# Kernel tuning notes

Hardware: AMD Instinct MI355X
Metric: run time of the kernel (lower is better)

Reference implementation:

```python
import jax, jax.numpy as jnp
import numpy as np

B = 128        # graph pairs per batch
NPG = 512      # nodes per graph (equal-size graphs -> dense batch is a reshape)
D = 64         # input feature dim
DEG = 16       # avg degree
FILTERS = [64, 32, 16]
RDIM = 10      # resize_dim
CCH = 8        # conv channels per similarity image
MLP = [32, 16, 8, 4, 1]


def _make_edges(rng, n_graphs, npg, deg):
    E = n_graphs * npg * deg
    off = np.repeat(np.arange(n_graphs, dtype=np.int64) * npg, npg * deg)
    src = rng.integers(0, npg, E) + off
    dst = rng.integers(0, npg, E) + off
    return jnp.asarray(np.stack([src, dst]), dtype=jnp.int32)


def setup_inputs() -> dict:
    key = jax.random.key(0)
    ks = jax.random.split(key, 40)
    rng = np.random.default_rng(0)
    N = B * NPG
    inp = {}
    inp['x_i'] = jax.random.normal(ks[0], (N, D), jnp.float32)
    inp['x_j'] = jax.random.normal(ks[1], (N, D), jnp.float32)
    # GCN weights
    dims = [D] + FILTERS
    k = 2
    for li in range(3):
        fi, fo = dims[li], dims[li + 1]
        inp[f'gcn_w{li}'] = jax.random.normal(ks[k], (fi, fo), jnp.float32) / np.sqrt(fi); k += 1
        inp[f'gcn_b{li}'] = jnp.zeros((fo,), jnp.float32)
    # Conv filters: one Conv2d(1->CCH, 3x3, SAME) per GNN layer, OIHW kernels
    for li in range(3):
        inp[f'conv_w{li}'] = jax.random.normal(ks[k], (CCH, 1, 3, 3), jnp.float32) / 3.0; k += 1
        inp[f'conv_b{li}'] = jnp.zeros((CCH,), jnp.float32)
    # MLP (Linear-ReLU stack) + scoring layer
    mdims = [3 * CCH * RDIM * RDIM] + MLP
    for li in range(len(MLP)):
        fi, fo = mdims[li], mdims[li + 1]
        inp[f'mlp_w{li}'] = jax.random.normal(ks[k], (fi, fo), jnp.float32) / np.sqrt(fi); k += 1
        inp[f'mlp_b{li}'] = jnp.zeros((fo,), jnp.float32)
    inp['score_w'] = jax.random.normal(ks[k], (1, 1), jnp.float32); k += 1
    inp['score_b'] = jnp.zeros((1,), jnp.float32)
    # Graph structure (int constants)
    inp['edge_index_i'] = _make_edges(rng, B, NPG, DEG)
    inp['edge_index_j'] = _make_edges(rng, B, NPG, DEG)
    batch = jnp.asarray(np.repeat(np.arange(B, dtype=np.int64), NPG), dtype=jnp.int32)
    inp['batch_i'] = batch
    inp['batch_j'] = batch
    return inp


def _gcn(x, ei, w, b):
    # PyG GCNConv: A_hat = D^-1/2 (A + I) D^-1/2 ; out = A_hat (x W) + b
    src, dst = ei[0], ei[1]
    n = x.shape[0]
    xw = x @ w
    deg = jax.ops.segment_sum(jnp.ones(ei.shape[1], xw.dtype), dst, num_segments=n) + 1.0
    inv = jax.lax.rsqrt(deg)
    msg = xw[src] * (inv[src] * inv[dst])[:, None]
    agg = jax.ops.segment_sum(msg, dst, num_segments=n)
    return agg + xw * (inv * inv)[:, None] + b


def _forward(x_i, x_j, gcn_w0, gcn_b0, gcn_w1, gcn_b1, gcn_w2, gcn_b2,
             conv_w0, conv_b0, conv_w1, conv_b1, conv_w2, conv_b2,
             mlp_w0, mlp_b0, mlp_w1, mlp_b1, mlp_w2, mlp_b2, mlp_w3, mlp_b3, mlp_w4, mlp_b4,
             score_w, score_b, edge_index_i, edge_index_j):
    gws = [(gcn_w0, gcn_b0), (gcn_w1, gcn_b1), (gcn_w2, gcn_b2)]
    cvs = [(conv_w0, conv_b0), (conv_w1, conv_b1), (conv_w2, conv_b2)]
    embs = []
    for li, (w, b) in enumerate(gws):
        x_i = _gcn(x_i, edge_index_i, w, b)
        x_j = _gcn(x_j, edge_index_j, w, b)
        if li != len(gws) - 1:  # activation + dropout (eval mode -> identity)
            x_i = jax.nn.relu(x_i)
            x_j = jax.nn.relu(x_j)
        h_i = x_i.reshape(B, NPG, -1)  # to_dense_batch (equal-size graphs)
        h_j = x_j.reshape(B, NPG, -1)
        sim = jnp.einsum('bnd,bmd->bnm', h_i, h_j)  # [B, NPG, NPG]
        simr = jax.image.resize(sim, (B, RDIM, RDIM), method='bilinear', antialias=False)
        cw, cb = cvs[li]
        y = jax.lax.conv_general_dilated(simr[:, None], cw, (1, 1), 'SAME')
        y = jax.nn.relu(y + cb[None, :, None, None])  # [B, CCH, RDIM, RDIM]
        embs.append(y.reshape(B, -1))
    feat = jnp.concatenate(embs, axis=1)  # [B, 3*CCH*RDIM*RDIM]
    for w, b in [(mlp_w0, mlp_b0), (mlp_w1, mlp_b1), (mlp_w2, mlp_b2), (mlp_w3, mlp_b3), (mlp_w4, mlp_b4)]:
        feat = jax.nn.relu(feat @ w + b)
    score = jax.nn.sigmoid(feat @ score_w + score_b)
    return score.reshape(-1)


def reference(x_i, x_j, gcn_w0, gcn_b0, gcn_w1, gcn_b1, gcn_w2, gcn_b2,
              conv_w0, conv_b0, conv_w1, conv_b1, conv_w2, conv_b2,
              mlp_w0, mlp_b0, mlp_w1, mlp_b1, mlp_w2, mlp_b2, mlp_w3, mlp_b3, mlp_w4, mlp_b4,
              score_w, score_b, edge_index_i, edge_index_j, batch_i, batch_j):
    # batch_i/batch_j are implicit in the block layout (equal-size graphs)
    return _forward(x_i, x_j, gcn_w0, gcn_b0, gcn_w1, gcn_b1, gcn_w2, gcn_b2,
                    conv_w0, conv_b0, conv_w1, conv_b1, conv_w2, conv_b2,
                    mlp_w0, mlp_b0, mlp_w1, mlp_b1, mlp_w2, mlp_b2, mlp_w3, mlp_b3, mlp_w4, mlp_b4,
                    score_w, score_b, edge_index_i, edge_index_j)
```

## Files before the change

kernel.cpp:

```cpp
#include <hip/hip_runtime.h>

typedef float fvec4 __attribute__((ext_vector_type(4)));

#define NN 65536
#define EE 1048576
#define BB 128
#define NPG 512
#define EPG 8192

__global__ __launch_bounds__(512)
void k_all(const float* __restrict__ x_i, const float* __restrict__ x_j,
           const float* __restrict__ gw0, const float* __restrict__ gb0,
           const float* __restrict__ gw1, const float* __restrict__ gb1,
           const float* __restrict__ gw2, const float* __restrict__ gb2,
           const int* __restrict__ ei, const int* __restrict__ ej,
           float* __restrict__ hs0, float* __restrict__ hs1, float* __restrict__ hs2) {
  __shared__ fvec4 bufA[NPG * 8];
  __shared__ fvec4 bufB[NPG * 8];
  __shared__ unsigned short sids[EPG];
  __shared__ int cnt[NPG];
  __shared__ int posb[NPG];
  __shared__ int nodeOf[NPG];
  __shared__ int bins[64];
  __shared__ int binpos[64];
  __shared__ int wsum[8];
  unsigned short* const dsts = reinterpret_cast<unsigned short*>(bufA);

  const int side = blockIdx.x >> 7;
  const int g = blockIdx.x & 127;
  const float* __restrict__ x = side ? x_j : x_i;
  const int* __restrict__ eidx = side ? ej : ei;
  const int v = threadIdx.x;
  const int base = g * NPG;
  const int ebase = g * EPG;

  cnt[v] = 0;
  if (v < 64) bins[v] = 0;
  __syncthreads();
  for (int k = v; k < EPG; k += 512) {
    int d = eidx[EE + ebase + k] - base;
    dsts[k] = (unsigned short)d;
    atomicAdd(&cnt[d], 1);
  }
  __syncthreads();

  const int count = cnt[v];
  const int deg = count > 63 ? 63 : count;
  atomicAdd(&bins[deg], 1);
  int xa = count;
  const int lane = v & 63;
#pragma unroll
  for (int d = 1; d < 64; d <<= 1) {
    int y = __shfl_up(xa, d, 64);
    if (lane >= d) xa += y;
  }
  const int wid = v >> 6;
  if (lane == 63) wsum[wid] = xa;
  __syncthreads();
  if (v < 64) {
    if (v == 0) {
      int a = 0;
#pragma unroll
      for (int i = 0; i < 8; ++i) { int tv = wsum[i]; wsum[i] = a; a += tv; }
    }
    int c = bins[v];
    int xb = c;
#pragma unroll
    for (int d = 1; d < 64; d <<= 1) {
      int y = __shfl_up(xb, d, 64);
      if (v >= d) xb += y;
    }
    binpos[v] = xb - c;
  }
  __syncthreads();
  const int start_v = xa - count + wsum[wid];
  posb[v] = start_v;
  {
    int rank = atomicAdd(&binpos[deg], 1);
    nodeOf[rank] = v;
  }
  __syncthreads();

  for (int k = v; k < EPG; k += 512) {
    int lv = eidx[ebase + k] - base;
    int p = atomicAdd(&posb[dsts[k]], 1);
    sids[p] = (unsigned short)((lv << 3) | (lv & 7));
  }
  __syncthreads();

  const int node = nodeOf[v];
  const int ncount = cnt[node];
  const int nstart = posb[node] - ncount;
  const float inv_v = rsqrtf((float)ncount + 1.0f);
  const int myKey = (node << 3) | (node & 7);

  constexpr int srows[20] = {25, 26, 76, 77, 127, 128, 178, 179, 229, 230,
                             281, 282, 332, 333, 383, 384, 434, 435, 485, 486};
  int slot = -1;
#pragma unroll
  for (int i = 0; i < 20; ++i)
    if (node == srows[i]) slot = i;
  const int hb = (side * BB + g) * 20;

  fvec4 a0[16];
#pragma unroll
  for (int q = 0; q < 16; ++q) a0[q] = fvec4{0.f, 0.f, 0.f, 0.f};
  {
    const fvec4* xv = reinterpret_cast<const fvec4*>(x + (size_t)(base + node) * 64);
#pragma unroll 1
    for (int k16 = 0; k16 < 4; ++k16) {
      fvec4 xq[4];
#pragma unroll
      for (int u = 0; u < 4; ++u) xq[u] = xv[4 * k16 + u];
#pragma unroll
      for (int u = 0; u < 4; ++u) {
#pragma unroll
        for (int j = 0; j < 4; ++j) {
          const float xk = xq[u][j];
          const fvec4* wr = reinterpret_cast<const fvec4*>(gw0 + (size_t)(16 * k16 + 4 * u + j) * 64);
#pragma unroll
          for (int q = 0; q < 16; ++q) a0[q] += xk * wr[q];
        }
      }
    }
  }

  fvec4 sA[8], sB[8];
#pragma unroll
  for (int q = 0; q < 8; ++q) {
    fvec4 mA = a0[q] * inv_v;
    fvec4 mB = a0[8 + q] * inv_v;
    bufA[myKey ^ q] = mA;
    bufB[myKey ^ q] = mB;
    sA[q] = mA;
    sB[q] = mB;
  }
  __syncthreads();

  {
    const int end = nstart + ncount;
    for (int e = nstart; e < end; ++e) {
      const int K = sids[e];
#pragma unroll
      for (int q = 0; q < 8; ++q) {
        const int idx = K ^ q;
        sA[q] += bufA[idx];
        sB[q] += bufB[idx];
      }
    }
  }

  fvec4 y1[8];
#pragma unroll
  for (int p = 0; p < 8; ++p) y1[p] = fvec4{0.f, 0.f, 0.f, 0.f};
  {
    const fvec4* gb0v = reinterpret_cast<const fvec4*>(gb0);
    fvec4* hp = reinterpret_cast<fvec4*>(hs0 + ((size_t)hb + slot) * 64);
#pragma unroll
    for (int q = 0; q < 16; ++q) {
      fvec4 s = (q < 8) ? sA[q] : sB[q - 8];
      fvec4 o = s * inv_v + gb0v[q];
#pragma unroll
      for (int j = 0; j < 4; ++j) o[j] = fmaxf(o[j], 0.f);
      if (slot >= 0) hp[q] = o;
#pragma unroll
      for (int j = 0; j < 4; ++j) {
        const float hf = o[j];
        const fvec4* wr = reinterpret_cast<const fvec4*>(gw1 + (size_t)(q * 4 + j) * 32);
#pragma unroll
        for (int p = 0; p < 8; ++p) y1[p] += hf * wr[p];
      }
    }
  }
  __syncthreads();

  fvec4 s1[8];
#pragma unroll
  for (int q = 0; q < 8; ++q) {
    fvec4 mv = y1[q] * inv_v;
    bufA[myKey ^ q] = mv;
    s1[q] = mv;
  }
  __syncthreads();
  {
    const int end = nstart + ncount;
    for (int e = nstart; e < end; ++e) {
      const int K = sids[e];
#pragma unroll
      for (int q = 0; q < 8; ++q) s1[q] += bufA[K ^ q];
    }
  }
  fvec4 y2[4];
#pragma unroll
  for (int p = 0; p < 4; ++p) y2[p] = fvec4{0.f, 0.f, 0.f, 0.f};
  {
    const fvec4* gb1v = reinterpret_cast<const fvec4*>(gb1);
    fvec4* hp = reinterpret_cast<fvec4*>(hs1 + ((size_t)hb + slot) * 32);
#pragma unroll
    for (int q = 0; q < 8; ++q) {
      fvec4 o = s1[q] * inv_v + gb1v[q];
#pragma unroll
      for (int j = 0; j < 4; ++j) o[j] = fmaxf(o[j], 0.f);
      if (slot >= 0) hp[q] = o;
#pragma unroll
      for (int j = 0; j < 4; ++j) {
        const float hf = o[j];
        const fvec4* wr = reinterpret_cast<const fvec4*>(gw2 + (size_t)(q * 4 + j) * 16);
#pragma unroll
        for (int p = 0; p < 4; ++p) y2[p] += hf * wr[p];
      }
    }
  }

  fvec4 s2[4];
#pragma unroll
  for (int q = 0; q < 4; ++q) {
    fvec4 mv = y2[q] * inv_v;
    bufB[myKey ^ q] = mv;
    s2[q] = mv;
  }
  __syncthreads();
  if (slot >= 0) {
    const int end = nstart + ncount;
    for (int e = nstart; e < end; ++e) {
      const int K = sids[e];
#pragma unroll
      for (int q = 0; q < 4; ++q) s2[q] += bufB[K ^ q];
    }
    const fvec4* gb2v = reinterpret_cast<const fvec4*>(gb2);
    fvec4* hp = reinterpret_cast<fvec4*>(hs2 + ((size_t)hb + slot) * 16);
#pragma unroll
    for (int q = 0; q < 4; ++q) hp[q] = s2[q] * inv_v + gb2v[q];
  }
}

__global__ __launch_bounds__(256) void k_head(const float* __restrict__ hs0, const float* __restrict__ hs1,
                                              const float* __restrict__ hs2,
                                              const float* __restrict__ cw0, const float* __restrict__ cb0,
                                              const float* __restrict__ cw1, const float* __restrict__ cb1,
                                              const float* __restrict__ cw2, const float* __restrict__ cb2,
                                              const float* __restrict__ mw0, const float* __restrict__ mb0,
                                              const float* __restrict__ mw1, const float* __restrict__ mb1,
                                              const float* __restrict__ mw2, const float* __restrict__ mb2,
                                              const float* __restrict__ mw3, const float* __restrict__ mb3,
                                              const float* __restrict__ mw4, const float* __restrict__ mb4,
                                              const float* __restrict__ sw, const float* __restrict__ sb,
                                              float* __restrict__ out) {
  __shared__ float hi[2240];
  __shared__ float hj[2240];
  __shared__ float sim[400];
  __shared__ float simr[100];
  __shared__ float feat[2400];
  __shared__ float red[256];
  __shared__ float mbuf[60];
  const int b = blockIdx.x, t = threadIdx.x;

  for (int k = t; k < 1280; k += 256) {
    hi[k] = hs0[(size_t)(0 * BB + b) * 1280 + k];
    hj[k] = hs0[(size_t)(1 * BB + b) * 1280 + k];
  }
  for (int k = t; k < 640; k += 256) {
    hi[1280 + k] = hs1[(size_t)(0 * BB + b) * 640 + k];
    hj[1280 + k] = hs1[(size_t)(1 * BB + b) * 640 + k];
  }
  for (int k = t; k < 320; k += 256) {
    hi[1920 + k] = hs2[(size_t)(0 * BB + b) * 320 + k];
    hj[1920 + k] = hs2[(size_t)(1 * BB + b) * 320 + k];
  }
  __syncthreads();

  const int Fs[3] = {64, 32, 16};
  const int HOFF[3] = {0, 1280, 1920};
  const float* CW[3] = {cw0, cw1, cw2};
  const float* CB[3] = {cb0, cb1, cb2};

  for (int li = 0; li < 3; ++li) {
    const int F = Fs[li];
    const float* Hi = hi + HOFF[li];
    const float* Hj = hj + HOFF[li];
    for (int p = t; p < 400; p += 256) {
      int r = p / 20, cq = p % 20;
      float a = 0.0f;
      for (int d = 0; d < F; ++d) a += Hi[r * F + d] * Hj[cq * F + d];
      sim[p] = a;
    }
    __syncthreads();
    if (t < 100) {
      int oy = t / 10, ox = t % 10;
      float cy = (oy + 0.5f) * (512.0f / 10.0f) - 0.5f;
      float cx = (ox + 0.5f) * (512.0f / 10.0f) - 0.5f;
      float fy = cy - floorf(cy);
      float fx = cx - floorf(cx);
      int r0 = 2 * oy, c0 = 2 * ox;
      float s00 = sim[r0 * 20 + c0], s01 = sim[r0 * 20 + c0 + 1];
      float s10 = sim[(r0 + 1) * 20 + c0], s11 = sim[(r0 + 1) * 20 + c0 + 1];
      simr[t] = (1.0f - fy) * ((1.0f - fx) * s00 + fx * s01) + fy * ((1.0f - fx) * s10 + fx * s11);
    }
    __syncthreads();
    const float* cw = CW[li];
    const float* cb = CB[li];
    for (int idx = t; idx < 800; idx += 256) {
      int cch = idx / 100, rem = idx % 100, y = rem / 10, x = rem % 10;
      float a = cb[cch];
#pragma unroll
      for (int ky = 0; ky < 3; ++ky) {
#pragma unroll
        for (int kx = 0; kx < 3; ++kx) {
          int iy = y + ky - 1, ix = x + kx - 1;
          if (iy >= 0 && iy < 10 && ix >= 0 && ix < 10)
            a += cw[cch * 9 + ky * 3 + kx] * simr[iy * 10 + ix];
        }
      }
      feat[li * 800 + idx] = fmaxf(a, 0.0f);
    }
    __syncthreads();
  }

  {
    int f = t & 31, part = t >> 5;
    float a = 0.0f;
    int k0 = part * 300;
    for (int k = k0; k < k0 + 300; ++k) a += feat[k] * mw0[k * 32 + f];
    red[t] = a;
    __syncthreads();
    if (t < 32) {
      float s = mb0[t];
#pragma unroll
      for (int p = 0; p < 8; ++p) s += red[p * 32 + t];
      mbuf[t] = fmaxf(s, 0.0f);
    }
    __syncthreads();
  }
  if (t < 16) {
    float s = mb1[t];
    for (int k = 0; k < 32; ++k) s += mbuf[k] * mw1[k * 16 + t];
    mbuf[32 + t] = fmaxf(s, 0.0f);
  }
  __syncthreads();
  if (t < 8) {
    float s = mb2[t];
    for (int k = 0; k < 16; ++k) s += mbuf[32 + k] * mw2[k * 8 + t];
    mbuf[48 + t] = fmaxf(s, 0.0f);
  }
  __syncthreads();
  if (t < 4) {
    float s = mb3[t];
    for (int k = 0; k < 8; ++k) s += mbuf[48 + k] * mw3[k * 4 + t];
    mbuf[56 + t] = fmaxf(s, 0.0f);
  }
  __syncthreads();
  if (t == 0) {
    float s = mb4[0];
    for (int k = 0; k < 4; ++k) s += mbuf[56 + k] * mw4[k];
    s = fmaxf(s, 0.0f);
    float z = s * sw[0] + sb[0];
    out[b] = 1.0f / (1.0f + expf(-z));
  }
}

extern "C" void kernel_launch(void* const* d_in, const int* in_sizes, int n_in,
                              void* d_out, int out_size, void* d_ws, size_t ws_size,
                              hipStream_t stream) {
  (void)in_sizes; (void)n_in; (void)out_size; (void)ws_size;
  const float* x_i = (const float*)d_in[0];
  const float* x_j = (const float*)d_in[1];
  const float* gw0 = (const float*)d_in[2];
  const float* gb0 = (const float*)d_in[3];
  const float* gw1 = (const float*)d_in[4];
  const float* gb1 = (const float*)d_in[5];
  const float* gw2 = (const float*)d_in[6];
  const float* gb2 = (const float*)d_in[7];
  const float* cw0 = (const float*)d_in[8];
  const float* cb0 = (const float*)d_in[9];
  const float* cw1 = (const float*)d_in[10];
  const float* cb1 = (const float*)d_in[11];
  const float* cw2 = (const float*)d_in[12];
  const float* cb2 = (const float*)d_in[13];
  const float* mw0 = (const float*)d_in[14];
  const float* mb0 = (const float*)d_in[15];
  const float* mw1 = (const float*)d_in[16];
  const float* mb1 = (const float*)d_in[17];
  const float* mw2 = (const float*)d_in[18];
  const float* mb2 = (const float*)d_in[19];
  const float* mw3 = (const float*)d_in[20];
  const float* mb3 = (const float*)d_in[21];
  const float* mw4 = (const float*)d_in[22];
  const float* mb4 = (const float*)d_in[23];
  const float* scw = (const float*)d_in[24];
  const float* scb = (const float*)d_in[25];
  const int* ei = (const int*)d_in[26];
  const int* ej = (const int*)d_in[27];
  float* out = (float*)d_out;

  char* p = (char*)d_ws;
  auto take = [&](size_t bytes) {
    char* r = p;
    p += (bytes + 255) & ~(size_t)255;
    return r;
  };
  float* hs0 = (float*)take((size_t)2 * BB * 20 * 64 * 4);
  float* hs1 = (float*)take((size_t)2 * BB * 20 * 32 * 4);
  float* hs2 = (float*)take((size_t)2 * BB * 20 * 16 * 4);

  k_all<<<2 * BB, 512, 0, stream>>>(x_i, x_j, gw0, gb0, gw1, gb1, gw2, gb2,
                                    ei, ej, hs0, hs1, hs2);
  k_head<<<BB, 256, 0, stream>>>(hs0, hs1, hs2, cw0, cb0, cw1, cb1, cw2, cb2,
                                 mw0, mb0, mw1, mb1, mw2, mb2, mw3, mb3, mw4, mb4,
                                 scw, scb, out);
}
```

Measured before the change: 132.6 us.

## Store GCN neighbor messages in LDS as packed fp16 and split layer-0 aggregation

The per-node feature messages kept in shared memory for neighbor aggregation are now packed as half2 pairs instead of fp32. This halves LDS footprint and read bandwidth per edge gather, and the swizzle key changes to match the smaller rows. Layer 0 is now aggregated in two 32-wide halves, one after the other, which lowers live register count, and the LDS write and sync for the second half are folded into the existing barrier. Accumulation stays in fp32, but each neighbor contribution is rounded to fp16, which adds numerical error against the fp32 reference.

```diff
diff --git a/kernel.cpp b/kernel.cpp
--- a/kernel.cpp
+++ b/kernel.cpp
@@ -1,12 +1,27 @@
 #include <hip/hip_runtime.h>
+#include <hip/hip_fp16.h>
 
 typedef float fvec4 __attribute__((ext_vector_type(4)));
+typedef int ivec4 __attribute__((ext_vector_type(4)));
 
 #define NN 65536
 #define EE 1048576
 #define BB 128
 #define NPG 512
 #define EPG 8192
+
+__device__ __forceinline__ int pkrtz(float a, float b) {
+  union { __half2 h; int i; } u; u.h = __floats2half2_rn(a, b); return u.i;
+}
+__device__ __forceinline__ float2 up2(int v) {
+  union { int i; __half2 h; } u; u.i = v; return __half22float2(u.h);
+}
+
+#define ACCQ(SA, SB, w) { float2 f_; \
+  f_ = up2((w)[0]); (SA)[0] += f_.x; (SA)[1] += f_.y; \
+  f_ = up2((w)[1]); (SA)[2] += f_.x; (SA)[3] += f_.y; \
+  f_ = up2((w)[2]); (SB)[0] += f_.x; (SB)[1] += f_.y; \
+  f_ = up2((w)[3]); (SB)[2] += f_.x; (SB)[3] += f_.y; }
 
 __global__ __launch_bounds__(512)
 void k_all(const float* __restrict__ x_i, const float* __restrict__ x_j,
@@ -15,8 +30,8 @@
            const float* __restrict__ gw2, const float* __restrict__ gb2,
            const int* __restrict__ ei, const int* __restrict__ ej,
            float* __restrict__ hs0, float* __restrict__ hs1, float* __restrict__ hs2) {
-  __shared__ fvec4 bufA[NPG * 8];
-  __shared__ fvec4 bufB[NPG * 8];
+  __shared__ ivec4 bufA[NPG * 4];
+  __shared__ ivec4 bufB[NPG * 4];
   __shared__ unsigned short sids[EPG];
   __shared__ int cnt[NPG];
   __shared__ int posb[NPG];
@@ -84,7 +99,7 @@
   for (int k = v; k < EPG; k += 512) {
     int lv = eidx[ebase + k] - base;
     int p = atomicAdd(&posb[dsts[k]], 1);
-    sids[p] = (unsigned short)((lv << 3) | (lv & 7));
+    sids[p] = (unsigned short)((lv << 2) | ((lv >> 1) & 3));
   }
   __syncthreads();
 
@@ -92,7 +107,7 @@
   const int ncount = cnt[node];
   const int nstart = posb[node] - ncount;
   const float inv_v = rsqrtf((float)ncount + 1.0f);
-  const int myKey = (node << 3) | (node & 7);
+  const int myKey = (node << 2) | ((node >> 1) & 3);
 
   constexpr int srows[20] = {25, 26, 76, 77, 127, 128, 178, 179, 229, 230,
                              281, 282, 332, 333, 383, 384, 434, 435, 485, 486};
@@ -125,15 +140,17 @@
     }
   }
 
-  fvec4 sA[8], sB[8];
-#pragma unroll
-  for (int q = 0; q < 8; ++q) {
-    fvec4 mA = a0[q] * inv_v;
-    fvec4 mB = a0[8 + q] * inv_v;
-    bufA[myKey ^ q] = mA;
-    bufB[myKey ^ q] = mB;
-    sA[q] = mA;
-    sB[q] = mB;
+  fvec4 s[8];
+#pragma unroll
+  for (int q = 0; q < 8; ++q) s[q] = a0[q] * inv_v;
+#pragma unroll
+  for (int q_ = 0; q_ < 4; ++q_) {
+    ivec4 w_;
+    w_[0] = pkrtz(s[2 * q_][0], s[2 * q_][1]);
+    w_[1] = pkrtz(s[2 * q_][2], s[2 * q_][3]);
+    w_[2] = pkrtz(s[2 * q_ + 1][0], s[2 * q_ + 1][1]);
+    w_[3] = pkrtz(s[2 * q_ + 1][2], s[2 * q_ + 1][3]);
+    bufA[myKey ^ q_] = w_;
   }
   __syncthreads();
 
@@ -141,13 +158,22 @@
     const int end = nstart + ncount;
     for (int e = nstart; e < end; ++e) {
       const int K = sids[e];
-#pragma unroll
-      for (int q = 0; q < 8; ++q) {
-        const int idx = K ^ q;
-        sA[q] += bufA[idx];
-        sB[q] += bufB[idx];
-      }
-    }
+      const ivec4 w0 = bufA[K], w1 = bufA[K ^ 1], w2 = bufA[K ^ 2], w3 = bufA[K ^ 3];
+      ACCQ(s[0], s[1], w0) ACCQ(s[2], s[3], w1) ACCQ(s[4], s[5], w2) ACCQ(s[6], s[7], w3)
+    }
+  }
+
+  fvec4 sB[8];
+#pragma unroll
+  for (int q = 0; q < 8; ++q) sB[q] = a0[8 + q] * inv_v;
+#pragma unroll
+  for (int q_ = 0; q_ < 4; ++q_) {
+    ivec4 w_;
+    w_[0] = pkrtz(sB[2 * q_][0], sB[2 * q_][1]);
+    w_[1] = pkrtz(sB[2 * q_][2], sB[2 * q_][3]);
+    w_[2] = pkrtz(sB[2 * q_ + 1][0], sB[2 * q_ + 1][1]);
+    w_[3] = pkrtz(sB[2 * q_ + 1][2], sB[2 * q_ + 1][3]);
+    bufB[myKey ^ q_] = w_;
   }
 
   fvec4 y1[8];
@@ -157,9 +183,8 @@
     const fvec4* gb0v = reinterpret_cast<const fvec4*>(gb0);
     fvec4* hp = reinterpret_cast<fvec4*>(hs0 + ((size_t)hb + slot) * 64);
 #pragma unroll
-    for (int q = 0; q < 16; ++q) {
-      fvec4 s = (q < 8) ? sA[q] : sB[q - 8];
-      fvec4 o = s * inv_v + gb0v[q];
+    for (int q = 0; q < 8; ++q) {
+      fvec4 o = s[q] * inv_v + gb0v[q];
 #pragma unroll
       for (int j = 0; j < 4; ++j) o[j] = fmaxf(o[j], 0.f);
       if (slot >= 0) hp[q] = o;
@@ -174,20 +199,53 @@
   }
   __syncthreads();
 
-  fvec4 s1[8];
-#pragma unroll
-  for (int q = 0; q < 8; ++q) {
-    fvec4 mv = y1[q] * inv_v;
-    bufA[myKey ^ q] = mv;
-    s1[q] = mv;
-  }
-  __syncthreads();
   {
     const int end = nstart + ncount;
     for (int e = nstart; e < end; ++e) {
       const int K = sids[e];
-#pragma unroll
-      for (int q = 0; q < 8; ++q) s1[q] += bufA[K ^ q];
+      const ivec4 w0 = bufB[K], w1 = bufB[K ^ 1], w2 = bufB[K ^ 2], w3 = bufB[K ^ 3];
+      ACCQ(sB[0], sB[1], w0) ACCQ(sB[2], sB[3], w1) ACCQ(sB[4], sB[5], w2) ACCQ(sB[6], sB[7], w3)
+    }
+  }
+  {
+    const fvec4* gb0v = reinterpret_cast<const fvec4*>(gb0);
+    fvec4* hp = reinterpret_cast<fvec4*>(hs0 + ((size_t)hb + slot) * 64);
+#pragma unroll
+    for (int q = 0; q < 8; ++q) {
+      fvec4 o = sB[q] * inv_v + gb0v[8 + q];
+#pragma unroll
+      for (int j = 0; j < 4; ++j) o[j] = fmaxf(o[j], 0.f);
+      if (slot >= 0) hp[8 + q] = o;
+#pragma unroll
+      for (int j = 0; j < 4; ++j) {
+        const float hf = o[j];
+        const fvec4* wr = reinterpret_cast<const fvec4*>(gw1 + (size_t)((8 + q) * 4 + j) * 32);
+#pragma unroll
+        for (int p = 0; p < 8; ++p) y1[p] += hf * wr[p];
+      }
+    }
+  }
+
+  fvec4 s1[8];
+#pragma unroll
+  for (int q = 0; q < 8; ++q) s1[q] = y1[q] * inv_v;
+#pragma unroll
+  for (int q_ = 0; q_ < 4; ++q_) {
+    ivec4 w_;
+    w_[0] = pkrtz(s1[2 * q_][0], s1[2 * q_][1]);
+    w_[1] = pkrtz(s1[2 * q_][2], s1[2 * q_][3]);
+    w_[2] = pkrtz(s1[2 * q_ + 1][0], s1[2 * q_ + 1][1]);
+    w_[3] = pkrtz(s1[2 * q_ + 1][2], s1[2 * q_ + 1][3]);
+    bufA[myKey ^ q_] = w_;
+  }
+  __syncthreads();
+
+  {
+    const int end = nstart + ncount;
+    for (int e = nstart; e < end; ++e) {
+      const int K = sids[e];
+      const ivec4 w0 = bufA[K], w1 = bufA[K ^ 1], w2 = bufA[K ^ 2], w3 = bufA[K ^ 3];
+      ACCQ(s1[0], s1[1], w0) ACCQ(s1[2], s1[3], w1) ACCQ(s1[4], s1[5], w2) ACCQ(s1[6], s1[7], w3)
     }
   }
   fvec4 y2[4];
@@ -214,18 +272,24 @@
 
   fvec4 s2[4];
 #pragma unroll
-  for (int q = 0; q < 4; ++q) {
-    fvec4 mv = y2[q] * inv_v;
-    bufB[myKey ^ q] = mv;
-    s2[q] = mv;
-  }
-  __syncthreads();
+  for (int q = 0; q < 4; ++q) s2[q] = y2[q] * inv_v;
+  {
+    ivec4 w0, w1;
+    w0[0] = pkrtz(s2[0][0], s2[0][1]); w0[1] = pkrtz(s2[0][2], s2[0][3]);
+    w0[2] = pkrtz(s2[1][0], s2[1][1]); w0[3] = pkrtz(s2[1][2], s2[1][3]);
+    w1[0] = pkrtz(s2[2][0], s2[2][1]); w1[1] = pkrtz(s2[2][2], s2[2][3]);
+    w1[2] = pkrtz(s2[3][0], s2[3][1]); w1[3] = pkrtz(s2[3][2], s2[3][3]);
+    bufB[myKey] = w0;
+    bufB[myKey ^ 1] = w1;
+  }
+  __syncthreads();
+
   if (slot >= 0) {
     const int end = nstart + ncount;
     for (int e = nstart; e < end; ++e) {
       const int K = sids[e];
-#pragma unroll
-      for (int q = 0; q < 4; ++q) s2[q] += bufB[K ^ q];
+      const ivec4 w0 = bufB[K], w1 = bufB[K ^ 1];
+      ACCQ(s2[0], s2[1], w0) ACCQ(s2[2], s2[3], w1)
     }
     const fvec4* gb2v = reinterpret_cast<const fvec4*>(gb2);
     fvec4* hp = reinterpret_cast<fvec4*>(hs2 + ((size_t)hb + slot) * 16);
```

Result: no change. 131.7 us (-0.7%).
